# Performance work log

Measured on AMD Instinct MI355X. Metric: run time of the kernel, lower is better.

The kernel has to match this reference:

```python
import jax, jax.numpy as jnp
import numpy as np

# Static cluster layout: B graphs, PER atoms each; first NIN are 'inside'
# (aux_ind==0), remaining NOUT are 'outside' periodic images (aux_ind==1).
B, PER, NIN, K = 256, 1024, 256, 32
NOUT = PER - NIN
N = B * PER
R = 6.0        # cutoff radius (Angstrom)
BOX = 32.0     # box side -> ~30 neighbors within R at this density


def setup_inputs() -> dict:
    key = jax.random.key(0)
    pos = jax.random.uniform(key, (N, 3), dtype=jnp.float32) * BOX
    batch = (jnp.arange(N, dtype=jnp.int32) // PER)
    aux_ind = ((jnp.arange(N, dtype=jnp.int32) % PER) >= NIN).astype(jnp.int32)
    return {"pos": pos, "batch": batch, "aux_ind": aux_ind}


def _select_neighbors(d, valid, k):
    """Pick up to k valid candidates per target, lowest candidate index first.
    d: [..., C] distances, valid: [..., C] bool. Returns (idx, mask, dist),
    each [..., k]; padded slots have mask=False and dist=0."""
    C = d.shape[-1]
    order_key = jnp.where(valid, jnp.arange(C, dtype=jnp.int32), C + 1)
    idx = jnp.argsort(order_key, axis=-1)[..., :k]          # [..., k]
    mask = jnp.take_along_axis(valid, idx, axis=-1)
    dist = jnp.where(mask, jnp.take_along_axis(d, idx, axis=-1), 0.0)
    return idx.astype(jnp.int32), mask, dist


def reference(pos, batch, aux_ind):
    # batch/aux_ind are encoded by the static contiguous layout above;
    # they parameterize the same structure torch builds via scatter_add/cumsum.
    pg = pos.reshape(B, PER, 3)
    ins = pg[:, :NIN]            # [B, NIN, 3]  inside (target + intra-conv) nodes
    outs = pg[:, NIN:]           # [B, NOUT, 3] outside (inter-conv) nodes

    # intra edges: inside -> inside, same graph, no self loops
    d_ii = jnp.sqrt(jnp.sum((ins[:, :, None, :] - ins[:, None, :, :]) ** 2, -1))  # [B,NIN,NIN]
    valid_ii = (d_ii < R) & ~jnp.eye(NIN, dtype=bool)
    idx_ii, m_ii, dist_ii = _select_neighbors(d_ii, valid_ii, K)

    # inter edges: outside -> inside, same graph
    d_io = jnp.sqrt(jnp.sum((ins[:, :, None, :] - outs[:, None, :, :]) ** 2, -1))  # [B,NIN,NOUT]
    valid_io = d_io < R
    idx_io, m_io, dist_io = _select_neighbors(d_io, valid_io, K)

    # relabel to global node indices (flow='source_to_target': row=source, col=target)
    goff = (jnp.arange(B, dtype=jnp.int32) * PER)[:, None, None]       # [B,1,1]
    tgt = jnp.broadcast_to(goff + jnp.arange(NIN, dtype=jnp.int32)[None, :, None],
                           (B, NIN, K))
    src_ii = goff + idx_ii
    src_io = goff + NIN + idx_io

    edge_index = jnp.stack([src_ii.reshape(-1), tgt.reshape(-1)], 0)        # [2, B*NIN*K]
    edge_index_inter = jnp.stack([src_io.reshape(-1), tgt.reshape(-1)], 0)  # [2, B*NIN*K]

    return (edge_index, m_ii.reshape(-1), dist_ii,
            edge_index_inter, m_io.reshape(-1), dist_io)
```

## Files before the change

### kernel.cpp

```cpp
#include <hip/hip_runtime.h>


constexpr int KK = 32;
constexpr unsigned EE = 2097152u;

typedef float v2f __attribute__((ext_vector_type(2)));

__device__ __forceinline__ v2f pk_add(v2f a, v2f b) {
    v2f d; asm("v_pk_add_f32 %0, %1, %2" : "=v"(d) : "v"(a), "v"(b)); return d;
}
__device__ __forceinline__ v2f pk_mul(v2f a, v2f b) {
    v2f d; asm("v_pk_mul_f32 %0, %1, %2" : "=v"(d) : "v"(a), "v"(b)); return d;
}

__device__ __forceinline__ int prefix_base(unsigned long long m, int base) {
    return __builtin_amdgcn_mbcnt_hi((unsigned)(m >> 32),
           __builtin_amdgcn_mbcnt_lo((unsigned)m, (unsigned)base));
}

__global__ __launch_bounds__(256) void mo3e_kernel(const float* __restrict__ pos,
                                                   float* __restrict__ out) {
    __shared__ float sq[3072];
    __shared__ int   slotrow[4][2][128];

    const int blk = blockIdx.x;
    const int b   = blk >> 5;
    const int tid = threadIdx.x;
    const int w   = tid >> 6;
    const int l   = tid & 63;
    const int i0  = __builtin_amdgcn_readfirstlane(((blk & 31) << 3) | (w << 1));

    {
        const float4* g4 = (const float4*)(pos + (size_t)b * 3072);
        float4* s4 = (float4*)sq;
        s4[tid      ] = g4[tid      ];
        s4[tid + 256] = g4[tid + 256];
        s4[tid + 512] = g4[tid + 512];
    }
    __syncthreads();

    const float x0 = sq[3 * i0],     y0 = sq[3 * i0 + 1], z0 = sq[3 * i0 + 2];
    const float x1 = sq[3 * i0 + 3], y1 = sq[3 * i0 + 4], z1 = sq[3 * i0 + 5];
    const v2f nx[2] = {{-x0, -x0}, {-x1, -x1}};
    const v2f ny[2] = {{-y0, -y0}, {-y1, -y1}};
    const v2f nz[2] = {{-z0, -z0}, {-z1, -z1}};

    int* const rows[2] = { slotrow[w][0], slotrow[w][1] };
    const int dump = 64 + l;
    const int gs   = i0 >> 6;
    const int sl   = i0 & 63;

    unsigned long long m0ii[2], m0io[2];
    int cii[2] = {0, 0};
    int cio[2] = {KK, KK};

    int av = 3 * l;
#pragma unroll
    for (int it = 0; it < 8; ++it) {
        const float xa = sq[av], ya = sq[av + 1], za = sq[av + 2];
        const float xb = sq[av + 192], yb = sq[av + 193], zb = sq[av + 194];
        av += 384;
        const v2f qx = {xa, xb}, qy = {ya, yb}, qz = {za, zb};
#pragma unroll
        for (int h = 0; h < 2; ++h) {
            const int g = 2 * it + h;
            const int idxv = (g << 6) | l;
#pragma unroll
            for (int T = 0; T < 2; ++T) {
                const v2f dx = pk_add(qx, nx[T]), dy = pk_add(qy, ny[T]),
                          dz = pk_add(qz, nz[T]);
                const v2f d2 = pk_add(pk_add(pk_mul(dx, dx), pk_mul(dy, dy)),
                                      pk_mul(dz, dz));
                const float dh = h ? d2.y : d2.x;
                bool pred = dh < 36.0f;
                unsigned long long ms = __ballot(pred);
                if (g == gs) {
                    ms &= ~(1ull << (sl + T));
                    pred = pred && (l != (sl + T));
                }
                if (g < 4) {
                    const int e = prefix_base(ms, cii[T]);
                    const bool wr = pred && (e < KK);
                    rows[T][wr ? e : dump] = idxv;
                    cii[T] += (int)__popcll(ms);
                    if (g == 0) m0ii[T] = ms;
                } else {
                    const int e = prefix_base(ms, cio[T]);
                    const bool wr = pred && (e < 2 * KK);
                    rows[T][wr ? e : dump] = idxv;
                    cio[T] += (int)__popcll(ms);
                    if (g == 4) m0io[T] = ms;
                }
            }
        }
    }

#pragma unroll
    for (int T = 0; T < 2; ++T) {
        if (cii[T] < KK) {
            const unsigned long long inv = ~m0ii[T];
            const int e = prefix_base(inv, cii[T]);
            const bool wr = ((inv >> l) & 1ull) && (e < KK);
            rows[T][wr ? e : dump] = l;
        }
        if (cio[T] < 2 * KK) {
            const unsigned long long inv = ~m0io[T];
            const int e = prefix_base(inv, cio[T]);
            const bool wr = ((inv >> l) & 1ull) && (e < 2 * KK);
            rows[T][wr ? e : dump] = 256 + l;
        }
    }

    const int goff = b << 10;
    float* const oSrc = out;
    float* const oTgt = out + EE;
    float* const oMsk = out + 2u * EE;
    float* const oDst = out + 3u * EE;
#pragma unroll
    for (int T = 0; T < 2; ++T) {
        const int idx = rows[T][l];
        const float qx = sq[3 * idx], qy = sq[3 * idx + 1], qz = sq[3 * idx + 2];
        const float xi = T ? x1 : x0, yi = T ? y1 : y0, zi = T ? z1 : z0;
        const float ddx = xi - qx, ddy = yi - qy, ddz = zi - qz;
        const float d2e = ddx * ddx + ddy * ddy + ddz * ddz;

        const bool isA = l < KK;
        const int  Sa  = cii[T] < KK ? cii[T] : KK;
        const int  Sb  = (cio[T] < 2 * KK ? cio[T] : 2 * KK) - KK;
        const bool mv  = (l & 31) < (isA ? Sa : Sb);
        const float dist = mv ? __builtin_amdgcn_sqrtf(d2e) : 0.0f;

        const unsigned e0  = (unsigned)((b << 8) + i0 + T) << 5;
        const unsigned off = (isA ? 0u : 4u * EE - 32u) + e0 + (unsigned)l;

        oSrc[off] = (float)(goff + idx);
        oTgt[off] = (float)(goff + i0 + T);
        oMsk[off] = mv ? 1.0f : 0.0f;
        oDst[off] = dist;
    }
}

extern "C" void kernel_launch(void* const* d_in, const int* in_sizes, int n_in,
                              void* d_out, int out_size, void* d_ws, size_t ws_size,
                              hipStream_t stream) {
    const float* pos = (const float*)d_in[0];
    float* out = (float*)d_out;

    mo3e_kernel<<<dim3(8192), dim3(256), 0, stream>>>(pos, out);
}
```

Before: 106.2 us.

## Process four target groups per block and store positions as packed SoA in LDS

Each block now handles 32 target atoms instead of 8, looping four rounds, so the per-graph position tile is loaded into shared memory once per four rounds rather than once per block, and the grid shrinks by four. Positions are transposed at load into separate x/y/z arrays interleaved as float2 pairs, so the candidate loop fetches packed pairs with single vector LDS reads instead of six strided scalar loads. The cost is fewer blocks for latency hiding and a more complex scatter at load time.

```diff
diff --git a/kernel.cpp b/kernel.cpp
--- a/kernel.cpp
+++ b/kernel.cpp
@@ -18,125 +18,144 @@
            __builtin_amdgcn_mbcnt_lo((unsigned)m, (unsigned)base));
 }
 
+__device__ __forceinline__ int fo_of(int j) {
+    return ((((j >> 7) << 6) | (j & 63)) << 1) | ((j >> 6) & 1);
+}
+
 __global__ __launch_bounds__(256) void mo3e_kernel(const float* __restrict__ pos,
                                                    float* __restrict__ out) {
-    __shared__ float sq[3072];
-    __shared__ int   slotrow[4][2][128];
+    __shared__ v2f sqx[512], sqy[512], sqz[512];
+    __shared__ int slotrow[4][2][128];
 
     const int blk = blockIdx.x;
-    const int b   = blk >> 5;
+    const int b   = blk >> 3;
     const int tid = threadIdx.x;
     const int w   = tid >> 6;
     const int l   = tid & 63;
-    const int i0  = __builtin_amdgcn_readfirstlane(((blk & 31) << 3) | (w << 1));
 
     {
         const float4* g4 = (const float4*)(pos + (size_t)b * 3072);
-        float4* s4 = (float4*)sq;
-        s4[tid      ] = g4[tid      ];
-        s4[tid + 256] = g4[tid + 256];
-        s4[tid + 512] = g4[tid + 512];
+        const float4 A = g4[3 * tid], Bq = g4[3 * tid + 1], C = g4[3 * tid + 2];
+        float* fx = (float*)sqx; float* fy = (float*)sqy; float* fz = (float*)sqz;
+        const float px[4] = {A.x, A.w, Bq.z, C.y};
+        const float py[4] = {A.y, Bq.x, Bq.w, C.z};
+        const float pz[4] = {A.z, Bq.y, C.x, C.w};
+#pragma unroll
+        for (int u = 0; u < 4; ++u) {
+            const int fo = fo_of(4 * tid + u);
+            fx[fo] = px[u]; fy[fo] = py[u]; fz[fo] = pz[u];
+        }
     }
     __syncthreads();
 
-    const float x0 = sq[3 * i0],     y0 = sq[3 * i0 + 1], z0 = sq[3 * i0 + 2];
-    const float x1 = sq[3 * i0 + 3], y1 = sq[3 * i0 + 4], z1 = sq[3 * i0 + 5];
-    const v2f nx[2] = {{-x0, -x0}, {-x1, -x1}};
-    const v2f ny[2] = {{-y0, -y0}, {-y1, -y1}};
-    const v2f nz[2] = {{-z0, -z0}, {-z1, -z1}};
-
+    const int goff = b << 10;
+    float* const oSrc = out;
+    float* const oTgt = out + EE;
+    float* const oMsk = out + 2u * EE;
+    float* const oDst = out + 3u * EE;
     int* const rows[2] = { slotrow[w][0], slotrow[w][1] };
     const int dump = 64 + l;
-    const int gs   = i0 >> 6;
-    const int sl   = i0 & 63;
 
-    unsigned long long m0ii[2], m0io[2];
-    int cii[2] = {0, 0};
-    int cio[2] = {KK, KK};
+    for (int R = 0; R < 4; ++R) {
+        const int i0 = __builtin_amdgcn_readfirstlane(
+            ((blk & 7) << 5) | (R << 3) | (w << 1));
 
-    int av = 3 * l;
+        const float x0 = ((float*)sqx)[fo_of(i0)];
+        const float y0 = ((float*)sqy)[fo_of(i0)];
+        const float z0 = ((float*)sqz)[fo_of(i0)];
+        const float x1 = ((float*)sqx)[fo_of(i0 + 1)];
+        const float y1 = ((float*)sqy)[fo_of(i0 + 1)];
+        const float z1 = ((float*)sqz)[fo_of(i0 + 1)];
+        const v2f nx[2] = {{-x0, -x0}, {-x1, -x1}};
+        const v2f ny[2] = {{-y0, -y0}, {-y1, -y1}};
+        const v2f nz[2] = {{-z0, -z0}, {-z1, -z1}};
+
+        const int gs = i0 >> 6;
+        const int sl = i0 & 63;
+
+        unsigned long long m0ii[2], m0io[2];
+        int cii[2] = {0, 0};
+        int cio[2] = {KK, KK};
+
 #pragma unroll
-    for (int it = 0; it < 8; ++it) {
-        const float xa = sq[av], ya = sq[av + 1], za = sq[av + 2];
-        const float xb = sq[av + 192], yb = sq[av + 193], zb = sq[av + 194];
-        av += 384;
-        const v2f qx = {xa, xb}, qy = {ya, yb}, qz = {za, zb};
-#pragma unroll
-        for (int h = 0; h < 2; ++h) {
-            const int g = 2 * it + h;
-            const int idxv = (g << 6) | l;
+        for (int p = 0; p < 8; ++p) {
+            const v2f qx = sqx[(p << 6) + l];
+            const v2f qy = sqy[(p << 6) + l];
+            const v2f qz = sqz[(p << 6) + l];
 #pragma unroll
             for (int T = 0; T < 2; ++T) {
                 const v2f dx = pk_add(qx, nx[T]), dy = pk_add(qy, ny[T]),
                           dz = pk_add(qz, nz[T]);
                 const v2f d2 = pk_add(pk_add(pk_mul(dx, dx), pk_mul(dy, dy)),
                                       pk_mul(dz, dz));
-                const float dh = h ? d2.y : d2.x;
-                bool pred = dh < 36.0f;
-                unsigned long long ms = __ballot(pred);
-                if (g == gs) {
-                    ms &= ~(1ull << (sl + T));
-                    pred = pred && (l != (sl + T));
-                }
-                if (g < 4) {
-                    const int e = prefix_base(ms, cii[T]);
-                    const bool wr = pred && (e < KK);
-                    rows[T][wr ? e : dump] = idxv;
-                    cii[T] += (int)__popcll(ms);
-                    if (g == 0) m0ii[T] = ms;
-                } else {
-                    const int e = prefix_base(ms, cio[T]);
-                    const bool wr = pred && (e < 2 * KK);
-                    rows[T][wr ? e : dump] = idxv;
-                    cio[T] += (int)__popcll(ms);
-                    if (g == 4) m0io[T] = ms;
+#pragma unroll
+                for (int h = 0; h < 2; ++h) {
+                    const int g = 2 * p + h;
+                    const int idxv = (g << 6) | l;
+                    const float dh = h ? d2.y : d2.x;
+                    bool pred = dh < 36.0f;
+                    unsigned long long ms = __ballot(pred);
+                    if (g == gs) {
+                        ms &= ~(1ull << (sl + T));
+                        pred = pred && (l != (sl + T));
+                    }
+                    if (g < 4) {
+                        const int e = prefix_base(ms, cii[T]);
+                        const bool wr = pred && (e < KK);
+                        rows[T][wr ? e : dump] = idxv;
+                        cii[T] += (int)__popcll(ms);
+                        if (g == 0) m0ii[T] = ms;
+                    } else {
+                        const int e = prefix_base(ms, cio[T]);
+                        const bool wr = pred && (e < 2 * KK);
+                        rows[T][wr ? e : dump] = idxv;
+                        cio[T] += (int)__popcll(ms);
+                        if (g == 4) m0io[T] = ms;
+                    }
                 }
             }
         }
-    }
 
 #pragma unroll
-    for (int T = 0; T < 2; ++T) {
-        if (cii[T] < KK) {
-            const unsigned long long inv = ~m0ii[T];
-            const int e = prefix_base(inv, cii[T]);
-            const bool wr = ((inv >> l) & 1ull) && (e < KK);
-            rows[T][wr ? e : dump] = l;
+        for (int T = 0; T < 2; ++T) {
+            if (cii[T] < KK) {
+                const unsigned long long inv = ~m0ii[T];
+                const int e = prefix_base(inv, cii[T]);
+                const bool wr = ((inv >> l) & 1ull) && (e < KK);
+                rows[T][wr ? e : dump] = l;
+            }
+            if (cio[T] < 2 * KK) {
+                const unsigned long long inv = ~m0io[T];
+                const int e = prefix_base(inv, cio[T]);
+                const bool wr = ((inv >> l) & 1ull) && (e < 2 * KK);
+                rows[T][wr ? e : dump] = 256 + l;
+            }
         }
-        if (cio[T] < 2 * KK) {
-            const unsigned long long inv = ~m0io[T];
-            const int e = prefix_base(inv, cio[T]);
-            const bool wr = ((inv >> l) & 1ull) && (e < 2 * KK);
-            rows[T][wr ? e : dump] = 256 + l;
+
+#pragma unroll
+        for (int T = 0; T < 2; ++T) {
+            const int idx = rows[T][l];
+            const int fg = fo_of(idx);
+            const float qx = ((float*)sqx)[fg], qy = ((float*)sqy)[fg],
+                        qz = ((float*)sqz)[fg];
+            const float xi = T ? x1 : x0, yi = T ? y1 : y0, zi = T ? z1 : z0;
+            const float ddx = xi - qx, ddy = yi - qy, ddz = zi - qz;
+            const float d2e = ddx * ddx + ddy * ddy + ddz * ddz;
+
+            const bool isA = l < KK;
+            const int  Sa  = cii[T] < KK ? cii[T] : KK;
+            const int  Sb  = (cio[T] < 2 * KK ? cio[T] : 2 * KK) - KK;
+            const bool mv  = (l & 31) < (isA ? Sa : Sb);
+            const float dist = mv ? __builtin_amdgcn_sqrtf(d2e) : 0.0f;
+
+            const unsigned e0  = (unsigned)((b << 8) + i0 + T) << 5;
+            const unsigned off = (isA ? 0u : 4u * EE - 32u) + e0 + (unsigned)l;
+
+            oSrc[off] = (float)(goff + idx);
+            oTgt[off] = (float)(goff + i0 + T);
+            oMsk[off] = mv ? 1.0f : 0.0f;
+            oDst[off] = dist;
         }
-    }
-
-    const int goff = b << 10;
-    float* const oSrc = out;
-    float* const oTgt = out + EE;
-    float* const oMsk = out + 2u * EE;
-    float* const oDst = out + 3u * EE;
-#pragma unroll
-    for (int T = 0; T < 2; ++T) {
-        const int idx = rows[T][l];
-        const float qx = sq[3 * idx], qy = sq[3 * idx + 1], qz = sq[3 * idx + 2];
-        const float xi = T ? x1 : x0, yi = T ? y1 : y0, zi = T ? z1 : z0;
-        const float ddx = xi - qx, ddy = yi - qy, ddz = zi - qz;
-        const float d2e = ddx * ddx + ddy * ddy + ddz * ddz;
-
-        const bool isA = l < KK;
-        const int  Sa  = cii[T] < KK ? cii[T] : KK;
-        const int  Sb  = (cio[T] < 2 * KK ? cio[T] : 2 * KK) - KK;
-        const bool mv  = (l & 31) < (isA ? Sa : Sb);
-        const float dist = mv ? __builtin_amdgcn_sqrtf(d2e) : 0.0f;
-
-        const unsigned e0  = (unsigned)((b << 8) + i0 + T) << 5;
-        const unsigned off = (isA ? 0u : 4u * EE - 32u) + e0 + (unsigned)l;
-
-        oSrc[off] = (float)(goff + idx);
-        oTgt[off] = (float)(goff + i0 + T);
-        oMsk[off] = mv ? 1.0f : 0.0f;
-        oDst[off] = dist;
     }
 }
 
@@ -146,5 +165,5 @@
     const float* pos = (const float*)d_in[0];
     float* out = (float*)d_out;
 
-    mo3e_kernel<<<dim3(8192), dim3(256), 0, stream>>>(pos, out);
+    mo3e_kernel<<<dim3(2048), dim3(256), 0, stream>>>(pos, out);
 }
```

Measured after the change: 112.8 us. 1.06x slower.
